# Performance work log

Measured on AMD Instinct MI355X. Metric: run time of the kernel, lower is better.

The kernel has to match this reference:

```python
import jax, jax.numpy as jnp
import numpy as np

B, N, D, H, DH = 4, 2048, 512, 8, 64  # batch, seqlen, hidden, heads, dim-per-head
EPS = 1e-5


def _layer_norm(x, g, b):
    m = jnp.mean(x, axis=-1, keepdims=True)
    v = jnp.var(x, axis=-1, keepdims=True)
    return (x - m) * jax.lax.rsqrt(v + EPS) * g + b


def setup_inputs() -> dict:
    key = jax.random.key(0)
    k0, k1, k2 = jax.random.split(key, 3)
    T = B * N
    return {
        "x": jax.random.normal(k0, (T, D), jnp.float32),
        "ln1_g": jnp.ones((D,), jnp.float32),
        "ln1_b": jnp.zeros((D,), jnp.float32),
        "w_uvqk": jax.random.normal(k1, (D, H * 4 * DH), jnp.float32) * 0.02,
        "ln2_g": jnp.ones((H * DH,), jnp.float32),
        "ln2_b": jnp.zeros((H * DH,), jnp.float32),
        "w_proj": jax.random.normal(k2, (H * DH, D), jnp.float32) * 0.02,
        "scaling_seqlen": N,
    }


def reference(x, ln1_g, ln1_b, w_uvqk, ln2_g, ln2_b, w_proj, scaling_seqlen):
    T = x.shape[0]
    # input layernorm -> fused uvqk projection -> SiLU
    normed_x = _layer_norm(x, ln1_g, ln1_b)
    silu_uvqk = jax.nn.silu(normed_x @ w_uvqk)          # [T, H*4*DH]
    silu_uvqk = silu_uvqk.reshape(T, H, 4 * DH)
    user, value, query, key = jnp.split(silu_uvqk, [DH, 2 * DH, 3 * DH], axis=-1)

    # jagged -> [B, N, H, DH] (equal-length sequences, offsets = i*N)
    q = query.reshape(B, N, H, DH)
    k = key.reshape(B, N, H, DH)
    v = value.reshape(B, N, H, DH)

    # HSTU attention: silu-gated (no softmax), causal, scaled by 1/scaling_seqlen
    scores = jnp.einsum('bnhd,bmhd->bhnm', q, k)        # [B, H, N, N]
    p = jax.nn.silu(scores) / jnp.float32(scaling_seqlen)
    causal = jnp.tril(jnp.ones((N, N), bool))
    p = jnp.where(causal, p, 0.0)
    attn = jnp.einsum('bhnm,bmhd->bnhd', p, v).reshape(T, H * DH)

    # output norm, user gate, projection, residual (dropout p=0.0 -> identity)
    normed_attn = _layer_norm(attn, ln2_g, ln2_b)
    user_flat = user.reshape(T, H * DH)
    out = (normed_attn * user_flat) @ w_proj + x
    return out
```

## Files before the change

kernel.cpp:

```cpp
#include <hip/hip_runtime.h>
#include <hip/hip_bf16.h>

typedef __bf16 bf16;
typedef __attribute__((ext_vector_type(8))) __bf16 bf16x8;
typedef __attribute__((ext_vector_type(4))) float f32x4;
typedef __attribute__((ext_vector_type(16))) float f32x16;

#define BB   4
#define NN   2048
#define DD   512
#define HH   8
#define DHH  64
#define TT   (BB*NN)
#define NUU  (HH*4*DHH)

#define AS1 __attribute__((address_space(1)))
#define AS3 __attribute__((address_space(3)))
__device__ __forceinline__ void gload16(const void* g, void* l){
  __builtin_amdgcn_global_load_lds((const AS1 void*)g, (AS3 void*)l, 16, 0, 0);
}

__device__ __forceinline__ float silu_fast(float x){
  return x * __builtin_amdgcn_rcpf(1.0f + __expf(-x));
}

__device__ __forceinline__ unsigned pk2(float a, float b){
  return (unsigned)__builtin_bit_cast(unsigned short, (bf16)a)
       | ((unsigned)__builtin_bit_cast(unsigned short, (bf16)b) << 16);
}

__device__ __forceinline__ void plswap(unsigned &a, unsigned &b){
  asm volatile("v_permlane32_swap_b32 %0, %1" : "+v"(a), "+v"(b));
}

__global__ void k_transpose2(const float* __restrict__ w1, bf16* __restrict__ o1,
                             const float* __restrict__ w2, bf16* __restrict__ o2){
  __shared__ float tile[32][33];
  int tx = threadIdx.x, ty = threadIdx.y;
  int bx = blockIdx.x;
  const float* in; bf16* out; int R, C, c0;
  if (bx < 64){ in = w1; out = o1; R = 512; C = 2048; c0 = bx*32; }
  else        { in = w2; out = o2; R = 512; C = 512;  c0 = (bx-64)*32; }
  int r0 = blockIdx.y*32;
  #pragma unroll
  for (int i=0;i<4;i++) tile[ty+i*8][tx] = in[(size_t)(r0+ty+i*8)*C + c0+tx];
  __syncthreads();
  #pragma unroll
  for (int i=0;i<4;i++) out[(size_t)(c0+ty+i*8)*R + r0+tx] = (bf16)tile[tx][ty+i*8];
}

__global__ void k_ln_cast(const float* __restrict__ x, const float* __restrict__ g,
                          const float* __restrict__ bta, bf16* __restrict__ out){
  int lane = threadIdx.x & 63;
  int row  = blockIdx.x*4 + (threadIdx.x>>6);
  const float* xr = x + (size_t)row*512 + lane*8;
  float4 v0 = *(const float4*)xr;
  float4 v1 = *(const float4*)(xr+4);
  float vv[8] = {v0.x,v0.y,v0.z,v0.w,v1.x,v1.y,v1.z,v1.w};
  float s = 0.f, ss = 0.f;
  #pragma unroll
  for (int j=0;j<8;j++){ s += vv[j]; ss += vv[j]*vv[j]; }
  #pragma unroll
  for (int d=32; d; d>>=1){ s += __shfl_xor(s,d); ss += __shfl_xor(ss,d); }
  float m  = s * (1.f/512.f);
  float vr = ss * (1.f/512.f) - m*m;
  float rs = rsqrtf(vr + 1e-5f);
  const float* gp = g + lane*8;
  const float* bp = bta + lane*8;
  bf16x8 o;
  #pragma unroll
  for (int j=0;j<8;j++) o[j] = (bf16)((vv[j]-m)*rs*gp[j] + bp[j]);
  *(bf16x8*)(out + (size_t)row*512 + lane*8) = o;
}

__global__ void k_ln_gate(const float* __restrict__ attn, const float* __restrict__ g,
                          const float* __restrict__ bta, const bf16* __restrict__ uvqk,
                          bf16* __restrict__ out){
  int lane = threadIdx.x & 63;
  int row  = blockIdx.x*4 + (threadIdx.x>>6);
  const float* xr = attn + (size_t)row*512 + lane*8;
  float4 v0 = *(const float4*)xr;
  float4 v1 = *(const float4*)(xr+4);
  float vv[8] = {v0.x,v0.y,v0.z,v0.w,v1.x,v1.y,v1.z,v1.w};
  float s = 0.f, ss = 0.f;
  #pragma unroll
  for (int j=0;j<8;j++){ s += vv[j]; ss += vv[j]*vv[j]; }
  #pragma unroll
  for (int d=32; d; d>>=1){ s += __shfl_xor(s,d); ss += __shfl_xor(ss,d); }
  float m  = s * (1.f/512.f);
  float vr = ss * (1.f/512.f) - m*m;
  float rs = rsqrtf(vr + 1e-5f);
  const float* gp = g + lane*8;
  const float* bp = bta + lane*8;
  const bf16* up = uvqk + (size_t)row*NUU + (lane>>3)*256 + ((lane*8)&63);
  bf16x8 uu = *(const bf16x8*)up;
  bf16x8 o;
  #pragma unroll
  for (int j=0;j<8;j++)
    o[j] = (bf16)(((vv[j]-m)*rs*gp[j] + bp[j]) * (float)uu[j]);
  *(bf16x8*)(out + (size_t)row*512 + lane*8) = o;
}

template<int EPI>
__global__ __launch_bounds__(256) void k_gemm(const bf16* __restrict__ A,
                                              const bf16* __restrict__ BT,
                                              int Nd, const float* __restrict__ resid,
                                              void* __restrict__ Cout,
                                              bf16* __restrict__ vtout){
  __shared__ __align__(16) char smem[32768];
  char* As = smem;
  char* Bs = smem + 16384;
  const int K = 512;
  int t = threadIdx.x, lane = t & 63, wid = t >> 6;
  int wr = wid >> 1, wc = wid & 1;
  int lin = blockIdx.x;
  int wk  = (lin & 7)*((int)gridDim.x >> 3) + (lin >> 3);
  int nx  = Nd >> 7;
  int m0 = (wk / nx) * 128, n0 = (wk % nx) * 128;
  int blk = (lane & 7) ^ (lane >> 3);
  const bf16* gA = A  + (size_t)(m0 + wid*32 + (lane>>3))*K + blk*8;
  const bf16* gB = BT + (size_t)(n0 + wid*32 + (lane>>3))*K + blk*8;
  f32x4 acc[4][4] = {};
  for (int k0 = 0; k0 < K; k0 += 64){
    __syncthreads();
    #pragma unroll
    for (int c = 0; c < 4; ++c){
      gload16(gA + (size_t)c*8*K, As + wid*4096 + c*1024);
      gload16(gB + (size_t)c*8*K, Bs + wid*4096 + c*1024);
    }
    gA += 64; gB += 64;
    __syncthreads();
    #pragma unroll
    for (int kk = 0; kk < 64; kk += 32){
      int c0 = kk + (lane >> 4) * 8;
      bf16x8 a[4], b[4];
      #pragma unroll
      for (int i = 0; i < 4; i++){
        int ra = wr*64 + i*16 + (lane & 15);
        a[i] = *(const bf16x8*)(As + (((ra*64 + c0)*2) ^ ((ra & 7) << 4)));
        int rb = wc*64 + i*16 + (lane & 15);
        b[i] = *(const bf16x8*)(Bs + (((rb*64 + c0)*2) ^ ((rb & 7) << 4)));
      }
      #pragma unroll
      for (int i = 0; i < 4; i++)
        #pragma unroll
        for (int jj = 0; jj < 4; jj++)
          acc[i][jj] = __builtin_amdgcn_mfma_f32_16x16x32_bf16(a[i], b[jj], acc[i][jj], 0, 0, 0);
    }
  }
  bool isv = (EPI == 0) && ((n0 & 255) == 0) && (wc == 1);
  #pragma unroll
  for (int i = 0; i < 4; i++){
    #pragma unroll
    for (int jj = 0; jj < 4; jj++){
      int col = n0 + wc*64 + jj*16 + (lane & 15);
      if (EPI == 0){
        union { unsigned long long u; ushort s[4]; } pw;
        #pragma unroll
        for (int r = 0; r < 4; r++){
          int rowg = m0 + wr*64 + i*16 + (lane >> 4)*4 + r;
          float sv = silu_fast(acc[i][jj][r]);
          ((bf16*)Cout)[(size_t)rowg*Nd + col] = (bf16)sv;
          pw.s[r] = __builtin_bit_cast(ushort, (bf16)sv);
        }
        if (isv){
          int dh    = jj*16 + (lane & 15);
          int rowg0 = m0 + wr*64 + i*16 + (lane >> 4)*4;
          int bb = rowg0 >> 11, nn = rowg0 & (NN-1);
          int hh = n0 >> 8;
          *(unsigned long long*)(vtout + ((size_t)((bb*HH + hh)*64 + dh)*NN + nn)) = pw.u;
        }
      } else {
        #pragma unroll
        for (int r = 0; r < 4; r++){
          int rowg = m0 + wr*64 + i*16 + (lane >> 4)*4 + r;
          ((float*)Cout)[(size_t)rowg*Nd + col] = acc[i][jj][r] + resid[(size_t)rowg*Nd + col];
        }
      }
    }
  }
}

__global__ __launch_bounds__(512) void k_attn(const bf16* __restrict__ uv,
                                              const bf16* __restrict__ vt,
                                              float* __restrict__ attn,
                                              const int* __restrict__ scal){
  __shared__ __align__(16) char smem[32768];
  int t = threadIdx.x, lane = t & 63, w = t >> 6;
  int hi5 = lane >> 5;
  int lin  = blockIdx.x;
  int work = (lin & 7)*80 + (lin >> 3);
  int grp  = work / 20;
  int d    = 19 - (work % 20);
  int b = grp >> 3, h = grp & 7;
  int qt, ch;
  if (d < 2)       { qt = d;               ch = 0; }
  else if (d < 6)  { qt = 2 + ((d-2)>>1);  ch = (d-2)&1; }
  else if (d < 12) { qt = 4 + (d-6)/3;     ch = (d-6)%3; }
  else             { qt = 6 + ((d-12)>>2); ch = (d-12)&3; }
  int total = 4*qt + 4;
  int nch   = (qt>>1) + 1;
  int bsz   = total / nch, rem = total - bsz*nch;
  int j0 = ch*bsz + (ch < rem ? ch : rem);
  int j1 = j0 + bsz + (ch < rem ? 1 : 0) - 1;
  int tok0 = b*NN + qt*256;
  float sinv = 1.0f / (float)(scal[0]);

  int blk  = (lane & 7) ^ (lane >> 3);
  int rsub = lane >> 3;

  bf16x8 qfrag[4];
  {
    const bf16* gq = uv + (size_t)(tok0 + w*32 + (lane & 31))*NUU + h*256 + 128 + hi5*8;
    #pragma unroll
    for (int ks = 0; ks < 4; ++ks)
      qfrag[ks] = *(const bf16x8*)(gq + ks*16);
  }
  const bf16* gk = uv + (size_t)(b*NN + j0*64 + w*8 + rsub)*NUU + h*256 + 192 + blk*8;
  const bf16* gv = vt + (size_t)((b*HH + h)*64 + w*8 + rsub)*NN + j0*64 + blk*8;
  gload16(gk, smem + w*1024);
  gload16(gv, smem + 8192 + w*1024);
  gk += (size_t)64*NUU; gv += 64;

  f32x16 oacc[2] = {};
  int qmin  = qt*256 + w*32;
  int qglob = qmin + (lane & 31);
  int cur = 0;
  for (int j = j0; j <= j1; ++j){
    asm volatile("s_waitcnt vmcnt(0)" ::: "memory");
    __builtin_amdgcn_s_barrier();
    if (j < j1){
      char* nb = smem + (cur^1)*16384;
      gload16(gk, nb + w*1024);
      gload16(gv, nb + 8192 + w*1024);
      gk += (size_t)64*NUU; gv += 64;
    }
    const char* Ks = smem + cur*16384;
    const char* Vs = Ks + 8192;
    #pragma unroll
    for (int sub = 0; sub < 2; ++sub){
      int kvbase = j*64 + sub*32;
      if (kvbase < qmin + 32){
        f32x16 sacc = {};
        int rk = sub*32 + (lane & 31);
        #pragma unroll
        for (int ks = 0; ks < 4; ++ks){
          int c0 = ks*16 + hi5*8;
          bf16x8 ak = *(const bf16x8*)(Ks + (((rk*64 + c0)*2) ^ ((rk & 7) << 4)));
          sacc = __builtin_amdgcn_mfma_f32_32x32x16_bf16(ak, qfrag[ks], sacc, 0, 0, 0);
        }
        union { unsigned u[8]; bf16x8 v[2]; } P;
        if (kvbase + 31 <= qmin){
          #pragma unroll
          for (int m = 0; m < 4; ++m){
            P.u[2*m]   = pk2(silu_fast(sacc[4*m+0]), silu_fast(sacc[4*m+1]));
            P.u[2*m+1] = pk2(silu_fast(sacc[4*m+2]), silu_fast(sacc[4*m+3]));
          }
        } else {
          #pragma unroll
          for (int m = 0; m < 4; ++m){
            float pr[4];
            #pragma unroll
            for (int r = 0; r < 4; ++r){
              int kvg = kvbase + 8*m + 4*hi5 + r;
              pr[r] = (kvg <= qglob) ? silu_fast(sacc[4*m+r]) : 0.0f;
            }
            P.u[2*m]   = pk2(pr[0], pr[1]);
            P.u[2*m+1] = pk2(pr[2], pr[3]);
          }
        }
        plswap(P.u[0], P.u[2]); plswap(P.u[1], P.u[3]);
        plswap(P.u[4], P.u[6]); plswap(P.u[5], P.u[7]);
        #pragma unroll
        for (int kh = 0; kh < 2; ++kh){
          int c0 = sub*32 + kh*16 + hi5*8;
          #pragma unroll
          for (int dsb = 0; dsb < 2; ++dsb){
            int rv = dsb*32 + (lane & 31);
            bf16x8 vb = *(const bf16x8*)(Vs + (((rv*64 + c0)*2) ^ ((rv & 7) << 4)));
            oacc[dsb] = __builtin_amdgcn_mfma_f32_32x32x16_bf16(P.v[kh], vb, oacc[dsb], 0, 0, 0);
          }
        }
      }
    }
    cur ^= 1;
  }
  #pragma unroll
  for (int dsb = 0; dsb < 2; ++dsb){
    #pragma unroll
    for (int r = 0; r < 16; ++r){
      int qrow = (r & 3) + 4*hi5 + 8*(r >> 2);
      atomicAdd(&attn[(size_t)(tok0 + w*32 + qrow)*DD + h*64 + dsb*32 + (lane & 31)],
                oacc[dsb][r] * sinv);
    }
  }
}

extern "C" void kernel_launch(void* const* d_in, const int* in_sizes, int n_in,
                              void* d_out, int out_size, void* d_ws, size_t ws_size,
                              hipStream_t stream){
  (void)in_sizes; (void)n_in; (void)out_size; (void)ws_size;
  const float* x      = (const float*)d_in[0];
  const float* ln1_g  = (const float*)d_in[1];
  const float* ln1_b  = (const float*)d_in[2];
  const float* w_uvqk = (const float*)d_in[3];
  const float* ln2_g  = (const float*)d_in[4];
  const float* ln2_b  = (const float*)d_in[5];
  const float* w_proj = (const float*)d_in[6];
  const int*   scal   = (const int*)d_in[7];
  float* out = (float*)d_out;

  char* ws = (char*)d_ws;
  bf16*  wT1  = (bf16*)(ws);
  bf16*  wT2  = (bf16*)(ws + (2u<<20));
  bf16*  xn   = (bf16*)(ws + (2u<<20) + (512u<<10));
  bf16*  uvq  = (bf16*)(ws + (10u<<20) + (512u<<10));
  float* attn = (float*)(ws + (42u<<20) + (512u<<10));
  bf16*  vtb  = (bf16*)(ws + (58u<<20) + (512u<<10));

  hipMemsetAsync(attn, 0, (size_t)TT*DD*sizeof(float), stream);
  k_transpose2<<<dim3(80,16), dim3(32,8), 0, stream>>>(w_uvqk, wT1, w_proj, wT2);
  k_ln_cast<<<TT/4, 256, 0, stream>>>(x, ln1_g, ln1_b, xn);
  k_gemm<0><<<dim3(1024), dim3(256), 0, stream>>>(xn, wT1, 2048, nullptr, (void*)uvq, vtb);
  k_attn<<<dim3(640), dim3(512), 0, stream>>>(uvq, vtb, attn, scal);
  k_ln_gate<<<TT/4, 256, 0, stream>>>(attn, ln2_g, ln2_b, uvq, xn);
  k_gemm<1><<<dim3(256), dim3(256), 0, stream>>>(xn, wT2, 512, x, (void*)out, nullptr);
}
```

Baseline: 116.5 us.

## Drop LDS staging in attention, load K/V fragments directly from global

The attention kernel stops staging K and V tiles in shared memory with a double-buffered global_load_lds pipeline and barriers. Each wave now reads its K and V MFMA fragments directly from global memory into registers. Blocks shrink to 4 waves covering 128 query rows with up to 8 KV tiles per chunk, giving 1280 blocks and a new causal work split, and each wave caps its KV loop at its own diagonal. This removes LDS traffic and barriers and improves load balance, but every wave now fetches K/V separately from global/L2, which loses the shared reuse across waves and exposes load latency without explicit prefetch.

```diff
diff --git a/kernel.cpp b/kernel.cpp
--- a/kernel.cpp
+++ b/kernel.cpp
@@ -181,74 +181,65 @@
   }
 }
 
-__global__ __launch_bounds__(512) void k_attn(const bf16* __restrict__ uv,
-                                              const bf16* __restrict__ vt,
-                                              float* __restrict__ attn,
-                                              const int* __restrict__ scal){
-  __shared__ __align__(16) char smem[32768];
+__global__ __launch_bounds__(256, 4) void k_attn(const bf16* __restrict__ uv,
+                                                 const bf16* __restrict__ vt,
+                                                 float* __restrict__ attn,
+                                                 const int* __restrict__ scal){
   int t = threadIdx.x, lane = t & 63, w = t >> 6;
   int hi5 = lane >> 5;
+  int l31 = lane & 31;
   int lin  = blockIdx.x;
-  int work = (lin & 7)*80 + (lin >> 3);
-  int grp  = work / 20;
-  int d    = 19 - (work % 20);
+  int work = (lin & 7)*160 + (lin >> 3);
+  int grp  = work / 40;
+  int d    = 39 - (work % 40);
   int b = grp >> 3, h = grp & 7;
   int qt, ch;
-  if (d < 2)       { qt = d;               ch = 0; }
-  else if (d < 6)  { qt = 2 + ((d-2)>>1);  ch = (d-2)&1; }
-  else if (d < 12) { qt = 4 + (d-6)/3;     ch = (d-6)%3; }
-  else             { qt = 6 + ((d-12)>>2); ch = (d-12)&3; }
-  int total = 4*qt + 4;
-  int nch   = (qt>>1) + 1;
-  int bsz   = total / nch, rem = total - bsz*nch;
-  int j0 = ch*bsz + (ch < rem ? ch : rem);
-  int j1 = j0 + bsz + (ch < rem ? 1 : 0) - 1;
-  int tok0 = b*NN + qt*256;
+  if (d < 4)       { qt = d;              ch = 0; }
+  else if (d < 12) { qt = 4  + (d-4)/2;   ch = (d-4)&1; }
+  else if (d < 24) { qt = 8  + (d-12)/3;  ch = (d-12)%3; }
+  else             { qt = 12 + (d-24)/4;  ch = (d-24)&3; }
+  int j0 = ch*8;
+  int jmax = 2*qt + 1;
+  int j1 = (jmax < j0+7) ? jmax : j0+7;
+  int tok0 = b*NN + qt*128;
   float sinv = 1.0f / (float)(scal[0]);
 
-  int blk  = (lane & 7) ^ (lane >> 3);
-  int rsub = lane >> 3;
+  int qmin  = qt*128 + w*32;
+  int qglob = qmin + l31;
+  int jw = (qmin + 31) >> 6;
+  if (jw < j1) j1 = jw;
 
   bf16x8 qfrag[4];
   {
-    const bf16* gq = uv + (size_t)(tok0 + w*32 + (lane & 31))*NUU + h*256 + 128 + hi5*8;
+    const bf16* gq = uv + (size_t)(tok0 + w*32 + l31)*NUU + h*256 + 128 + hi5*8;
     #pragma unroll
     for (int ks = 0; ks < 4; ++ks)
       qfrag[ks] = *(const bf16x8*)(gq + ks*16);
   }
-  const bf16* gk = uv + (size_t)(b*NN + j0*64 + w*8 + rsub)*NUU + h*256 + 192 + blk*8;
-  const bf16* gv = vt + (size_t)((b*HH + h)*64 + w*8 + rsub)*NN + j0*64 + blk*8;
-  gload16(gk, smem + w*1024);
-  gload16(gv, smem + 8192 + w*1024);
-  gk += (size_t)64*NUU; gv += 64;
+  const bf16* gK = uv + (size_t)(b*NN)*NUU + h*256 + 192 + hi5*8;
+  const bf16* gV = vt + (size_t)((b*HH + h)*64 + l31)*NN + hi5*8;
 
   f32x16 oacc[2] = {};
-  int qmin  = qt*256 + w*32;
-  int qglob = qmin + (lane & 31);
-  int cur = 0;
   for (int j = j0; j <= j1; ++j){
-    asm volatile("s_waitcnt vmcnt(0)" ::: "memory");
-    __builtin_amdgcn_s_barrier();
-    if (j < j1){
-      char* nb = smem + (cur^1)*16384;
-      gload16(gk, nb + w*1024);
-      gload16(gv, nb + 8192 + w*1024);
-      gk += (size_t)64*NUU; gv += 64;
-    }
-    const char* Ks = smem + cur*16384;
-    const char* Vs = Ks + 8192;
     #pragma unroll
     for (int sub = 0; sub < 2; ++sub){
       int kvbase = j*64 + sub*32;
       if (kvbase < qmin + 32){
+        const bf16* kp = gK + (size_t)(kvbase + l31)*NUU;
+        bf16x8 kf[4];
+        #pragma unroll
+        for (int ks = 0; ks < 4; ++ks)
+          kf[ks] = *(const bf16x8*)(kp + ks*16);
         f32x16 sacc = {};
-        int rk = sub*32 + (lane & 31);
-        #pragma unroll
-        for (int ks = 0; ks < 4; ++ks){
-          int c0 = ks*16 + hi5*8;
-          bf16x8 ak = *(const bf16x8*)(Ks + (((rk*64 + c0)*2) ^ ((rk & 7) << 4)));
-          sacc = __builtin_amdgcn_mfma_f32_32x32x16_bf16(ak, qfrag[ks], sacc, 0, 0, 0);
-        }
+        #pragma unroll
+        for (int ks = 0; ks < 4; ++ks)
+          sacc = __builtin_amdgcn_mfma_f32_32x32x16_bf16(kf[ks], qfrag[ks], sacc, 0, 0, 0);
+        bf16x8 vf[2][2];
+        #pragma unroll
+        for (int kh = 0; kh < 2; ++kh)
+          #pragma unroll
+          for (int dsb = 0; dsb < 2; ++dsb)
+            vf[kh][dsb] = *(const bf16x8*)(gV + (size_t)(dsb*32)*NN + kvbase + kh*16);
         union { unsigned u[8]; bf16x8 v[2]; } P;
         if (kvbase + 31 <= qmin){
           #pragma unroll
@@ -272,25 +263,19 @@
         plswap(P.u[0], P.u[2]); plswap(P.u[1], P.u[3]);
         plswap(P.u[4], P.u[6]); plswap(P.u[5], P.u[7]);
         #pragma unroll
-        for (int kh = 0; kh < 2; ++kh){
-          int c0 = sub*32 + kh*16 + hi5*8;
+        for (int kh = 0; kh < 2; ++kh)
           #pragma unroll
-          for (int dsb = 0; dsb < 2; ++dsb){
-            int rv = dsb*32 + (lane & 31);
-            bf16x8 vb = *(const bf16x8*)(Vs + (((rv*64 + c0)*2) ^ ((rv & 7) << 4)));
-            oacc[dsb] = __builtin_amdgcn_mfma_f32_32x32x16_bf16(P.v[kh], vb, oacc[dsb], 0, 0, 0);
-          }
-        }
+          for (int dsb = 0; dsb < 2; ++dsb)
+            oacc[dsb] = __builtin_amdgcn_mfma_f32_32x32x16_bf16(P.v[kh], vf[kh][dsb], oacc[dsb], 0, 0, 0);
       }
     }
-    cur ^= 1;
   }
   #pragma unroll
   for (int dsb = 0; dsb < 2; ++dsb){
     #pragma unroll
     for (int r = 0; r < 16; ++r){
       int qrow = (r & 3) + 4*hi5 + 8*(r >> 2);
-      atomicAdd(&attn[(size_t)(tok0 + w*32 + qrow)*DD + h*64 + dsb*32 + (lane & 31)],
+      atomicAdd(&attn[(size_t)(tok0 + w*32 + qrow)*DD + h*64 + dsb*32 + l31],
                 oacc[dsb][r] * sinv);
     }
   }
@@ -322,7 +307,7 @@
   k_transpose2<<<dim3(80,16), dim3(32,8), 0, stream>>>(w_uvqk, wT1, w_proj, wT2);
   k_ln_cast<<<TT/4, 256, 0, stream>>>(x, ln1_g, ln1_b, xn);
   k_gemm<0><<<dim3(1024), dim3(256), 0, stream>>>(xn, wT1, 2048, nullptr, (void*)uvq, vtb);
-  k_attn<<<dim3(640), dim3(512), 0, stream>>>(uvq, vtb, attn, scal);
+  k_attn<<<dim3(1280), dim3(256), 0, stream>>>(uvq, vtb, attn, scal);
   k_ln_gate<<<TT/4, 256, 0, stream>>>(attn, ln2_g, ln2_b, uvq, xn);
   k_gemm<1><<<dim3(256), dim3(256), 0, stream>>>(xn, wT2, 512, x, (void*)out, nullptr);
 }
```

After: 153.4 us. 31.7% more time.

## Rework attention split into 128-row tiles with two-way KV split, drop atomics

Applied to the files above, without the earlier changes.

Attention work is re-partitioned into 128-query tiles with 256-thread blocks. Long tiles are split into at most two KV chunks using a constant lookup table for load balance. Each chunk writes to its own buffer with plain stores, which replaces atomicAdd and the memset; the layer-norm kernel sums the two partials for the later rows. The KV prefetch is also issued before the barrier with a partial vmcnt wait, plus a trailing barrier, so loads overlap compute.

```diff
diff --git a/kernel.cpp b/kernel.cpp
--- a/kernel.cpp
+++ b/kernel.cpp
@@ -32,6 +32,15 @@
 __device__ __forceinline__ void plswap(unsigned &a, unsigned &b){
   asm volatile("v_permlane32_swap_b32 %0, %1" : "+v"(a), "+v"(b));
 }
+
+__constant__ unsigned ATBL[24] = {
+  7u|(0u<<4)|(16u<<10), 15u|(0u<<4)|(16u<<10), 14u|(0u<<4)|(15u<<10), 14u|(15u<<4)|(15u<<10),
+  6u|(0u<<4)|(14u<<10), 13u|(0u<<4)|(14u<<10), 12u|(0u<<4)|(13u<<10), 11u|(0u<<4)|(12u<<10),
+  15u|(16u<<4)|(16u<<10), 13u|(14u<<4)|(14u<<10), 12u|(13u<<4)|(13u<<10), 10u|(0u<<4)|(11u<<10),
+  10u|(11u<<4)|(11u<<10), 9u|(0u<<4)|(10u<<10), 5u|(0u<<4)|(12u<<10), 11u|(12u<<4)|(12u<<10),
+  0u|(0u<<4)|(2u<<10), 1u|(0u<<4)|(4u<<10), 2u|(0u<<4)|(6u<<10), 3u|(0u<<4)|(8u<<10),
+  8u|(0u<<4)|(9u<<10), 9u|(10u<<4)|(10u<<10), 8u|(9u<<4)|(9u<<10), 4u|(0u<<4)|(10u<<10)
+};
 
 __global__ void k_transpose2(const float* __restrict__ w1, bf16* __restrict__ o1,
                              const float* __restrict__ w2, bf16* __restrict__ o2){
@@ -73,15 +82,22 @@
   *(bf16x8*)(out + (size_t)row*512 + lane*8) = o;
 }
 
-__global__ void k_ln_gate(const float* __restrict__ attn, const float* __restrict__ g,
-                          const float* __restrict__ bta, const bf16* __restrict__ uvqk,
-                          bf16* __restrict__ out){
+__global__ void k_ln_gate(const float* __restrict__ attn0, const float* __restrict__ attn1,
+                          const float* __restrict__ g, const float* __restrict__ bta,
+                          const bf16* __restrict__ uvqk, bf16* __restrict__ out){
   int lane = threadIdx.x & 63;
   int row  = blockIdx.x*4 + (threadIdx.x>>6);
-  const float* xr = attn + (size_t)row*512 + lane*8;
+  const float* xr = attn0 + (size_t)row*512 + lane*8;
   float4 v0 = *(const float4*)xr;
   float4 v1 = *(const float4*)(xr+4);
   float vv[8] = {v0.x,v0.y,v0.z,v0.w,v1.x,v1.y,v1.z,v1.w};
+  if (((row & (NN-1)) >> 7) >= 8){
+    const float* x2 = attn1 + (size_t)row*512 + lane*8;
+    float4 w0 = *(const float4*)x2;
+    float4 w1 = *(const float4*)(x2+4);
+    vv[0]+=w0.x; vv[1]+=w0.y; vv[2]+=w0.z; vv[3]+=w0.w;
+    vv[4]+=w1.x; vv[5]+=w1.y; vv[6]+=w1.z; vv[7]+=w1.w;
+  }
   float s = 0.f, ss = 0.f;
   #pragma unroll
   for (int j=0;j<8;j++){ s += vv[j]; ss += vv[j]*vv[j]; }
@@ -181,29 +197,26 @@
   }
 }
 
-__global__ __launch_bounds__(512) void k_attn(const bf16* __restrict__ uv,
-                                              const bf16* __restrict__ vt,
-                                              float* __restrict__ attn,
-                                              const int* __restrict__ scal){
+__global__ __launch_bounds__(256, 4) void k_attn(const bf16* __restrict__ uv,
+                                                 const bf16* __restrict__ vt,
+                                                 float* __restrict__ attn0,
+                                                 float* __restrict__ attn1,
+                                                 const int* __restrict__ scal){
   __shared__ __align__(16) char smem[32768];
   int t = threadIdx.x, lane = t & 63, w = t >> 6;
   int hi5 = lane >> 5;
-  int lin  = blockIdx.x;
-  int work = (lin & 7)*80 + (lin >> 3);
-  int grp  = work / 20;
-  int d    = 19 - (work % 20);
+  int l31 = lane & 31;
+  int lin = blockIdx.x;
+  int pos = lin & 255;
+  int grp = pos & 31;
+  int rank = (lin >> 8)*8 + (pos >> 5);
+  unsigned e = ATBL[rank];
+  int qt = e & 15;
+  int j0 = (int)((e >> 4) & 63);
+  int j1 = j0 + (int)(e >> 10) - 1;
+  float* ob = j0 ? attn1 : attn0;
   int b = grp >> 3, h = grp & 7;
-  int qt, ch;
-  if (d < 2)       { qt = d;               ch = 0; }
-  else if (d < 6)  { qt = 2 + ((d-2)>>1);  ch = (d-2)&1; }
-  else if (d < 12) { qt = 4 + (d-6)/3;     ch = (d-6)%3; }
-  else             { qt = 6 + ((d-12)>>2); ch = (d-12)&3; }
-  int total = 4*qt + 4;
-  int nch   = (qt>>1) + 1;
-  int bsz   = total / nch, rem = total - bsz*nch;
-  int j0 = ch*bsz + (ch < rem ? ch : rem);
-  int j1 = j0 + bsz + (ch < rem ? 1 : 0) - 1;
-  int tok0 = b*NN + qt*256;
+  int tok0 = b*NN + qt*128;
   float sinv = 1.0f / (float)(scal[0]);
 
   int blk  = (lane & 7) ^ (lane >> 3);
@@ -211,30 +224,35 @@
 
   bf16x8 qfrag[4];
   {
-    const bf16* gq = uv + (size_t)(tok0 + w*32 + (lane & 31))*NUU + h*256 + 128 + hi5*8;
+    const bf16* gq = uv + (size_t)(tok0 + w*32 + l31)*NUU + h*256 + 128 + hi5*8;
     #pragma unroll
     for (int ks = 0; ks < 4; ++ks)
       qfrag[ks] = *(const bf16x8*)(gq + ks*16);
   }
-  const bf16* gk = uv + (size_t)(b*NN + j0*64 + w*8 + rsub)*NUU + h*256 + 192 + blk*8;
-  const bf16* gv = vt + (size_t)((b*HH + h)*64 + w*8 + rsub)*NN + j0*64 + blk*8;
-  gload16(gk, smem + w*1024);
-  gload16(gv, smem + 8192 + w*1024);
+  const bf16* gk = uv + (size_t)(b*NN + j0*64 + w*16 + rsub)*NUU + h*256 + 192 + blk*8;
+  const bf16* gv = vt + (size_t)((b*HH + h)*64 + w*16 + rsub)*NN + j0*64 + blk*8;
+  gload16(gk,                  smem + w*2048);
+  gload16(gk + (size_t)8*NUU,  smem + w*2048 + 1024);
+  gload16(gv,                  smem + 8192 + w*2048);
+  gload16(gv + (size_t)8*NN,   smem + 8192 + w*2048 + 1024);
   gk += (size_t)64*NUU; gv += 64;
 
   f32x16 oacc[2] = {};
-  int qmin  = qt*256 + w*32;
-  int qglob = qmin + (lane & 31);
+  int qmin  = qt*128 + w*32;
+  int qglob = qmin + l31;
   int cur = 0;
   for (int j = j0; j <= j1; ++j){
-    asm volatile("s_waitcnt vmcnt(0)" ::: "memory");
+    if (j < j1){
+      gload16(gk,                 smem + (cur^1)*16384 + w*2048);
+      gload16(gk + (size_t)8*NUU, smem + (cur^1)*16384 + w*2048 + 1024);
+      gload16(gv,                 smem + (cur^1)*16384 + 8192 + w*2048);
+      gload16(gv + (size_t)8*NN,  smem + (cur^1)*16384 + 8192 + w*2048 + 1024);
+      gk += (size_t)64*NUU; gv += 64;
+      asm volatile("s_waitcnt vmcnt(4)" ::: "memory");
+    } else {
+      asm volatile("s_waitcnt vmcnt(0)" ::: "memory");
+    }
     __builtin_amdgcn_s_barrier();
-    if (j < j1){
-      char* nb = smem + (cur^1)*16384;
-      gload16(gk, nb + w*1024);
-      gload16(gv, nb + 8192 + w*1024);
-      gk += (size_t)64*NUU; gv += 64;
-    }
     const char* Ks = smem + cur*16384;
     const char* Vs = Ks + 8192;
     #pragma unroll
@@ -242,7 +260,7 @@
       int kvbase = j*64 + sub*32;
       if (kvbase < qmin + 32){
         f32x16 sacc = {};
-        int rk = sub*32 + (lane & 31);
+        int rk = sub*32 + l31;
         #pragma unroll
         for (int ks = 0; ks < 4; ++ks){
           int c0 = ks*16 + hi5*8;
@@ -276,13 +294,15 @@
           int c0 = sub*32 + kh*16 + hi5*8;
           #pragma unroll
           for (int dsb = 0; dsb < 2; ++dsb){
-            int rv = dsb*32 + (lane & 31);
+            int rv = dsb*32 + l31;
             bf16x8 vb = *(const bf16x8*)(Vs + (((rv*64 + c0)*2) ^ ((rv & 7) << 4)));
             oacc[dsb] = __builtin_amdgcn_mfma_f32_32x32x16_bf16(P.v[kh], vb, oacc[dsb], 0, 0, 0);
           }
         }
       }
     }
+    asm volatile("" ::: "memory");
+    __builtin_amdgcn_s_barrier();
     cur ^= 1;
   }
   #pragma unroll
@@ -290,8 +310,7 @@
     #pragma unroll
     for (int r = 0; r < 16; ++r){
       int qrow = (r & 3) + 4*hi5 + 8*(r >> 2);
-      atomicAdd(&attn[(size_t)(tok0 + w*32 + qrow)*DD + h*64 + dsb*32 + (lane & 31)],
-                oacc[dsb][r] * sinv);
+      ob[(size_t)(tok0 + w*32 + qrow)*DD + h*64 + dsb*32 + l31] = oacc[dsb][r] * sinv;
     }
   }
 }
@@ -317,12 +336,12 @@
   bf16*  uvq  = (bf16*)(ws + (10u<<20) + (512u<<10));
   float* attn = (float*)(ws + (42u<<20) + (512u<<10));
   bf16*  vtb  = (bf16*)(ws + (58u<<20) + (512u<<10));
-
-  hipMemsetAsync(attn, 0, (size_t)TT*DD*sizeof(float), stream);
+  float* attn1= (float*)(ws + (66u<<20) + (512u<<10));
+
   k_transpose2<<<dim3(80,16), dim3(32,8), 0, stream>>>(w_uvqk, wT1, w_proj, wT2);
   k_ln_cast<<<TT/4, 256, 0, stream>>>(x, ln1_g, ln1_b, xn);
   k_gemm<0><<<dim3(1024), dim3(256), 0, stream>>>(xn, wT1, 2048, nullptr, (void*)uvq, vtb);
-  k_attn<<<dim3(640), dim3(512), 0, stream>>>(uvq, vtb, attn, scal);
-  k_ln_gate<<<TT/4, 256, 0, stream>>>(attn, ln2_g, ln2_b, uvq, xn);
+  k_attn<<<dim3(768), dim3(256), 0, stream>>>(uvq, vtb, attn, attn1, scal);
+  k_ln_gate<<<TT/4, 256, 0, stream>>>(attn, attn1, ln2_g, ln2_b, uvq, xn);
   k_gemm<1><<<dim3(256), dim3(256), 0, stream>>>(xn, wT2, 512, x, (void*)out, nullptr);
 }
```

Result: faster. 98.61 us (-15.3%).
